# Kernel tuning notes

Measured on AMD Instinct MI355X. Metric: run time of the kernel, lower is better.

## Reference

```python
import jax, jax.numpy as jnp
import numpy as np

N = 50000
E = 800000
D_IN = 128
D_HID = 256


def setup_inputs() -> dict:
    key = jax.random.key(0)
    ks = jax.random.split(key, 9)
    x = jax.random.normal(ks[0], (N, D_IN), dtype=jnp.float32)
    edge_index = jax.random.randint(ks[1], (2, E), 0, N, dtype=jnp.int64)
    edge_weight = jax.random.uniform(ks[2], (E,), dtype=jnp.float32)
    # GCNConv params (lin: y = x @ W.T, plus bias added after aggregation)
    W1 = jax.random.normal(ks[3], (D_HID, D_IN), dtype=jnp.float32) / np.sqrt(D_IN)
    b1 = jnp.zeros((D_HID,), dtype=jnp.float32)
    W2 = jax.random.normal(ks[4], (D_IN, D_HID), dtype=jnp.float32) / np.sqrt(D_HID)
    b2 = jnp.zeros((D_IN,), dtype=jnp.float32)
    gamma = jnp.ones((D_IN,), dtype=jnp.float32)
    beta = jnp.zeros((D_IN,), dtype=jnp.float32)
    return {"x": x, "edge_index": edge_index, "edge_weight": edge_weight,
            "W1": W1, "b1": b1, "W2": W2, "b2": b2,
            "gamma": gamma, "beta": beta}


def _gcn_norm(edge_index, edge_weight, n_nodes):
    # add self loops with weight 1.0 (PyG gcn_norm default)
    loop = jnp.arange(n_nodes, dtype=edge_index.dtype)
    src = jnp.concatenate([edge_index[0], loop])
    dst = jnp.concatenate([edge_index[1], loop])
    w = jnp.concatenate([edge_weight, jnp.ones((n_nodes,), edge_weight.dtype)])
    # symmetric normalization: deg over target index
    deg = jax.ops.segment_sum(w, dst, num_segments=n_nodes)
    dinv = jnp.where(deg > 0, jax.lax.rsqrt(deg), 0.0)
    norm = dinv[src] * w * dinv[dst]
    return src, dst, norm


def _gcn_conv(x, src, dst, norm, W, b, n_nodes):
    h = x @ W.T                                    # [N, out]
    msg = h[src] * norm[:, None]                   # gather + scale [E+N, out]
    out = jax.ops.segment_sum(msg, dst, num_segments=n_nodes)
    return out + b


def reference(x, edge_index, edge_weight, W1, b1, W2, b2, gamma, beta):
    n_nodes = x.shape[0]
    src, dst, norm = _gcn_norm(edge_index, edge_weight, n_nodes)
    h = _gcn_conv(x, src, dst, norm, W1, b1, n_nodes)
    h = jax.nn.relu(h)
    h = _gcn_conv(h, src, dst, norm, W2, b2, n_nodes)
    # LayerNorm over last dim
    mu = jnp.mean(h, axis=-1, keepdims=True)
    var = jnp.mean(jnp.square(h - mu), axis=-1, keepdims=True)
    h = (h - mu) * jax.lax.rsqrt(var + 1e-5) * gamma + beta
    return h
```

## Files before the change

kernel.cpp:

```cpp
#include <hip/hip_runtime.h>

typedef unsigned short ushort_t;
typedef unsigned long long u64_t;
typedef __attribute__((ext_vector_type(8))) short short8;
typedef __attribute__((ext_vector_type(4))) float float4v;

__device__ inline float b2f(ushort_t u) {
    unsigned x = ((unsigned)u) << 16;
    return __builtin_bit_cast(float, x);
}
__device__ inline ushort_t f2b(float f) {
    unsigned x = __builtin_bit_cast(unsigned, f);
    unsigned r = (x + 0x7fffu + ((x >> 16) & 1u)) >> 16;
    return (ushort_t)r;
}

__device__ inline void load_edge(const int* __restrict__ ei, int e, int E,
                                 int& s, int& d) {
    int ec = min(e, E - 1);
    int2 c64 = ((const int2*)ei)[ec];
    unsigned long long m = __ballot(c64.y != 0);
    if (m != 0ull) {
        s = ei[ec];
        d = ei[(size_t)E + ec];
    } else {
        s = c64.x;
        d = ((const int2*)ei)[(size_t)E + ec].x;
    }
}


__global__ __launch_bounds__(256) void k_mega(const int* __restrict__ ei,
                                              const float* __restrict__ w,
                                              const float* __restrict__ x,
                                              const float* __restrict__ W1,
                                              const float* __restrict__ W2,
                                              u64_t* packed, int* __restrict__ rank,
                                              ushort_t* __restrict__ xb,
                                              ushort_t* __restrict__ W1b,
                                              ushort_t* __restrict__ W2b,
                                              int E, int Nn, int gE, int gX) {
    int b = blockIdx.x;
    if (b < gE) {
        int e = b * 256 + threadIdx.x;
        int s, d;
        load_edge(ei, e, E, s, d);
        if (e < E) {
            if ((unsigned)s < (unsigned)Nn && (unsigned)d < (unsigned)Nn) {
                unsigned fx = (unsigned)(w[e] * 16777216.0f + 0.5f);
                u64_t old = atomicAdd(packed + d, (1ull << 32) | (u64_t)fx);
                rank[e] = (int)(old >> 32);
            } else {
                rank[e] = -1;
            }
        }
    } else if (b < gE + gX) {
        int i = (b - gE) * 256 + threadIdx.x;
        if (i < Nn * 32) {
            float4v v = ((const float4v*)x)[i];
            ushort4 o;
            o.x = f2b(v[0]); o.y = f2b(v[1]); o.z = f2b(v[2]); o.w = f2b(v[3]);
            ((ushort4*)xb)[i] = o;
        }
    } else {
        int i = (b - gE - gX) * 256 + threadIdx.x;
        if (i < 32768) W1b[i] = f2b(W1[i]);
        else if (i < 65536) W2b[i - 32768] = f2b(W2[i - 32768]);
    }
}

__device__ inline int cnt_hi(const u64_t* packed, int i) {
    return ((const int*)packed)[2 * i + 1];
}


__global__ __launch_bounds__(256) void k_scan_a(const u64_t* __restrict__ packed,
                                                int* __restrict__ bsum, int Nn) {
    int b = blockIdx.x, t = threadIdx.x;
    int base = b * 2048 + t * 8;
    int s = 0;
#pragma unroll
    for (int j = 0; j < 8; ++j) { int i = base + j; if (i < Nn) s += cnt_hi(packed, i); }
#pragma unroll
    for (int off = 1; off < 64; off <<= 1) s += __shfl_xor(s, off);
    __shared__ int wsum[4];
    if ((t & 63) == 0) wsum[t >> 6] = s;
    __syncthreads();
    if (t == 0) bsum[b] = wsum[0] + wsum[1] + wsum[2] + wsum[3];
}

__global__ void k_scan_b(const int* __restrict__ bsum, int* __restrict__ bbase,
                         int nb, int* __restrict__ offs, int Nn) {
    int t = threadIdx.x;
    int own = (t < nb) ? bsum[t] : 0;
    int v = own;
#pragma unroll
    for (int off = 1; off < 64; off <<= 1) {
        int u = __shfl_up(v, off);
        if (t >= off) v += u;
    }
    if (t < nb) bbase[t] = v - own;
    if (t == 63) offs[Nn] = v;
}

__global__ __launch_bounds__(256) void k_scan_c(const u64_t* __restrict__ packed,
                                                const int* __restrict__ bbase,
                                                int* __restrict__ offs,
                                                float* __restrict__ dinv, int Nn) {
    int b = blockIdx.x, t = threadIdx.x;
    int base = b * 2048 + t * 8;
    u64_t pk[8];
    int v[8];
    int s = 0;
#pragma unroll
    for (int j = 0; j < 8; ++j) {
        int i = base + j;
        pk[j] = (i < Nn) ? packed[i] : 0ull;
        v[j] = (int)(pk[j] >> 32);
        s += v[j];
    }
    __shared__ int sd[256];
    sd[t] = s;
    __syncthreads();
    for (int off = 1; off < 256; off <<= 1) {
        int u = (t >= off) ? sd[t - off] : 0;
        __syncthreads();
        sd[t] += u;
        __syncthreads();
    }
    int pos = bbase[b] + sd[t] - s;
#pragma unroll
    for (int j = 0; j < 8; ++j) {
        int i = base + j;
        if (i < Nn) {
            offs[i] = pos; pos += v[j];
            float deg = 1.0f + (float)(unsigned)(pk[j] & 0xFFFFFFFFull) * (1.0f / 16777216.0f);
            dinv[i] = rsqrtf(deg);
        }
    }
}


__global__ void k_scatter(const int* __restrict__ ei, const float* __restrict__ w,
                          const float* __restrict__ dinv,
                          const int* __restrict__ offs,
                          const int* __restrict__ rank,
                          int2* __restrict__ edata, int E, int Nn) {
    int e = blockIdx.x * 256 + threadIdx.x;
    int s, d;
    load_edge(ei, e, E, s, d);
    if (e >= E) return;
    int r = rank[e];
    if (r < 0) return;
    int pos = offs[d] + r;
    float nw = dinv[s] * w[e] * dinv[d];
    int2 p;
    p.x = s;
    p.y = __builtin_bit_cast(int, nw);
    edata[pos] = p;
}


__device__ inline void agg_edges(const ushort_t* __restrict__ src,
                                 const int2* __restrict__ edata,
                                 int s, int e, int hl, int p, float* a) {
    int i = s;
    for (; i + 7 < e; i += 8) {
#pragma unroll
        for (int j = 0; j < 4; ++j) {
            int idx = i + p + 2 * j;
            int2 ed = edata[idx];
            float nw = __builtin_bit_cast(float, ed.y);
            ushort4 q = ((const ushort4*)(src + (size_t)ed.x * 128))[hl];
            a[0] += b2f(q.x) * nw; a[1] += b2f(q.y) * nw;
            a[2] += b2f(q.z) * nw; a[3] += b2f(q.w) * nw;
        }
    }
    for (; i < e; i += 2) {
        int idx = i + p;
        int ic = min(idx, e - 1);
        int2 ed = edata[ic];
        float nw = (idx < e) ? __builtin_bit_cast(float, ed.y) : 0.f;
        ushort4 q = ((const ushort4*)(src + (size_t)ed.x * 128))[hl];
        a[0] += b2f(q.x) * nw; a[1] += b2f(q.y) * nw;
        a[2] += b2f(q.z) * nw; a[3] += b2f(q.w) * nw;
    }
}

__global__ __launch_bounds__(256) void k_agg1(const ushort_t* __restrict__ xb,
                                              const int* __restrict__ offs,
                                              const int2* __restrict__ edata,
                                              const float* __restrict__ dinv,
                                              ushort_t* __restrict__ ax, int Nn) {
    int v = (blockIdx.x * blockDim.x + threadIdx.x) >> 6;
    int lane = threadIdx.x & 63;
    if (v >= Nn) return;
    int hl = lane & 31, p = lane >> 5;
    float a[4] = {0.f, 0.f, 0.f, 0.f};
    if (p == 0) {
        float dv = dinv[v];
        float sn = dv * dv;
        ushort4 pq = ((const ushort4*)(xb + (size_t)v * 128))[hl];
        a[0] = b2f(pq.x) * sn; a[1] = b2f(pq.y) * sn;
        a[2] = b2f(pq.z) * sn; a[3] = b2f(pq.w) * sn;
    }
    int s = offs[v], e = offs[v + 1];
    agg_edges(xb, edata, s, e, hl, p, a);
#pragma unroll
    for (int j = 0; j < 4; ++j) a[j] += __shfl_xor(a[j], 32);
    if (p == 0) {
        ushort4 o;
        o.x = f2b(a[0]); o.y = f2b(a[1]); o.z = f2b(a[2]); o.w = f2b(a[3]);
        ((ushort4*)(ax + (size_t)v * 128))[hl] = o;
    }
}


__global__ __launch_bounds__(256, 2) void k_gemm_fused(const ushort_t* __restrict__ ax,
                                                       const ushort_t* __restrict__ W1b,
                                                       const float* __restrict__ b1v,
                                                       const ushort_t* __restrict__ W2b,
                                                       ushort_t* __restrict__ h2, int Nn) {
    __shared__ ushort_t tile[64][264];
    int tid = threadIdx.x, wid = tid >> 6, lane = tid & 63;
    int m = lane & 15, q = lane >> 4;
    int blk = blockIdx.x * 64;

    short8 wf[4][4];
#pragma unroll
    for (int nt = 0; nt < 4; ++nt) {
        const ushort_t* wb = W1b + (size_t)(wid * 64 + nt * 16 + m) * 128 + q * 8;
#pragma unroll
        for (int kt = 0; kt < 4; ++kt) wf[nt][kt] = *(const short8*)(wb + kt * 32);
    }
    short8 af[4][4];
#pragma unroll
    for (int mi = 0; mi < 4; ++mi) {
        int arow = blk + mi * 16 + m;
        bool rv = arow < Nn;
        const ushort_t* ab = ax + (size_t)arow * 128 + q * 8;
#pragma unroll
        for (int kt = 0; kt < 4; ++kt)
            af[mi][kt] = rv ? *(const short8*)(ab + kt * 32) : (short8)0;
    }

    float4v acc1[4][4];
#pragma unroll
    for (int mi = 0; mi < 4; ++mi)
#pragma unroll
        for (int nt = 0; nt < 4; ++nt) acc1[mi][nt] = (float4v){0.f, 0.f, 0.f, 0.f};

#pragma unroll
    for (int kt = 0; kt < 4; ++kt)
#pragma unroll
        for (int mi = 0; mi < 4; ++mi)
#pragma unroll
            for (int nt = 0; nt < 4; ++nt)
                acc1[mi][nt] = __builtin_amdgcn_mfma_f32_16x16x32_bf16(
                    af[mi][kt], wf[nt][kt], acc1[mi][nt], 0, 0, 0);

#pragma unroll
    for (int nt = 0; nt < 4; ++nt) {
        int col = wid * 64 + nt * 16 + m;
        float bb = b1v[col];
#pragma unroll
        for (int mi = 0; mi < 4; ++mi) {
#pragma unroll
            for (int r = 0; r < 4; ++r) {
                float v = acc1[mi][nt][r] + bb;
                v = v > 0.f ? v : 0.f;
                tile[mi * 16 + q * 4 + r][col] = f2b(v);
            }
        }
    }
    __syncthreads();

    short8 w2f[2][8];
#pragma unroll
    for (int n2 = 0; n2 < 2; ++n2) {
        const ushort_t* wb = W2b + (size_t)(wid * 32 + n2 * 16 + m) * 256 + q * 8;
#pragma unroll
        for (int kt = 0; kt < 8; ++kt) w2f[n2][kt] = *(const short8*)(wb + kt * 32);
    }

    float4v acc2[4][2];
#pragma unroll
    for (int mi = 0; mi < 4; ++mi)
#pragma unroll
        for (int n2 = 0; n2 < 2; ++n2) acc2[mi][n2] = (float4v){0.f, 0.f, 0.f, 0.f};

#pragma unroll
    for (int kt = 0; kt < 8; ++kt) {
#pragma unroll
        for (int mi = 0; mi < 4; ++mi) {
            short8 a2 = *(const short8*)&tile[mi * 16 + m][kt * 32 + q * 8];
#pragma unroll
            for (int n2 = 0; n2 < 2; ++n2)
                acc2[mi][n2] = __builtin_amdgcn_mfma_f32_16x16x32_bf16(
                    a2, w2f[n2][kt], acc2[mi][n2], 0, 0, 0);
        }
    }

#pragma unroll
    for (int mi = 0; mi < 4; ++mi) {
#pragma unroll
        for (int n2 = 0; n2 < 2; ++n2) {
            int col = wid * 32 + n2 * 16 + m;
#pragma unroll
            for (int r = 0; r < 4; ++r) {
                int row = blk + mi * 16 + q * 4 + r;
                if (row < Nn) h2[(size_t)row * 128 + col] = f2b(acc2[mi][n2][r]);
            }
        }
    }
}


__global__ __launch_bounds__(256) void k_agg2_ln(const ushort_t* __restrict__ h2,
                                                 const int* __restrict__ offs,
                                                 const int2* __restrict__ edata,
                                                 const float* __restrict__ dinv,
                                                 const float* __restrict__ b2v,
                                                 const float* __restrict__ gv,
                                                 const float* __restrict__ bev,
                                                 float* __restrict__ out, int Nn) {
    int v = (blockIdx.x * blockDim.x + threadIdx.x) >> 6;
    int lane = threadIdx.x & 63;
    if (v >= Nn) return;
    int hl = lane & 31, p = lane >> 5;
    float a[4] = {0.f, 0.f, 0.f, 0.f};
    if (p == 0) {
        float dv = dinv[v];
        float sn = dv * dv;
        ushort4 pq = ((const ushort4*)(h2 + (size_t)v * 128))[hl];
        a[0] = b2f(pq.x) * sn; a[1] = b2f(pq.y) * sn;
        a[2] = b2f(pq.z) * sn; a[3] = b2f(pq.w) * sn;
    }
    int s = offs[v], e = offs[v + 1];
    agg_edges(h2, edata, s, e, hl, p, a);
#pragma unroll
    for (int j = 0; j < 4; ++j) a[j] += __shfl_xor(a[j], 32);

    int d0 = hl * 4;
#pragma unroll
    for (int j = 0; j < 4; ++j) a[j] += b2v[d0 + j];

    float ssum = a[0] + a[1] + a[2] + a[3];
    float ssq = a[0] * a[0] + a[1] * a[1] + a[2] * a[2] + a[3] * a[3];
#pragma unroll
    for (int off = 1; off < 64; off <<= 1) {
        ssum += __shfl_xor(ssum, off);
        ssq += __shfl_xor(ssq, off);
    }
    float mu = ssum * (1.0f / 256.0f);
    float var = ssq * (1.0f / 256.0f) - mu * mu;
    float r = rsqrtf(var + 1e-5f);
    if (p == 0) {
        float4v o;
#pragma unroll
        for (int j = 0; j < 4; ++j)
            o[j] = (a[j] - mu) * r * gv[d0 + j] + bev[d0 + j];
        ((float4v*)(out + (size_t)v * 128))[hl] = o;
    }
}


extern "C" void kernel_launch(void* const* d_in, const int* in_sizes, int n_in,
                              void* d_out, int out_size, void* d_ws, size_t ws_size,
                              hipStream_t stream) {
    const float* x   = (const float*)d_in[0];
    const int*   ei  = (const int*)d_in[1];
    const float* ew  = (const float*)d_in[2];
    const float* W1  = (const float*)d_in[3];
    const float* b1v = (const float*)d_in[4];
    const float* W2  = (const float*)d_in[5];
    const float* b2v = (const float*)d_in[6];
    const float* gv  = (const float*)d_in[7];
    const float* bev = (const float*)d_in[8];
    float* out = (float*)d_out;

    const int Nn = in_sizes[0] / 128;
    const int E  = in_sizes[2];

    char* base = (char*)d_ws;
    size_t off = 0;
    auto alloc = [&](size_t bytes) {
        char* p = base + off;
        off = (off + bytes + 255) & ~(size_t)255;
        return p;
    };
    u64_t*  packed = (u64_t*)alloc((size_t)Nn * 8);
    float*  dinv   = (float*)alloc((size_t)Nn * 4);
    int*    offs   = (int*)alloc((size_t)(Nn + 1) * 4);
    int*    bsum   = (int*)alloc(64 * 4);
    int*    bbase  = (int*)alloc(64 * 4);
    int*    rank   = (int*)alloc((size_t)E * 4);
    int2*   edata  = (int2*)alloc((size_t)E * 8);
    ushort_t* xb   = (ushort_t*)alloc((size_t)Nn * 128 * 2);
    ushort_t* h2   = (ushort_t*)alloc((size_t)Nn * 128 * 2);
    ushort_t* W1b  = (ushort_t*)alloc(32768 * 2);
    ushort_t* W2b  = (ushort_t*)alloc(32768 * 2);
    ushort_t* ax   = (ushort_t*)d_out;
    (void)ws_size; (void)n_in; (void)out_size;

    int gE = (E + 255) / 256;
    int gX = (Nn * 32 + 255) / 256;
    int gW = (Nn + 3) / 4;
    int gG = (Nn + 63) / 64;
    int nb = (Nn + 2047) / 2048;

    hipMemsetAsync(packed, 0, (size_t)Nn * 8, stream);
    k_mega<<<gE + gX + 256, 256, 0, stream>>>(ei, ew, x, W1, W2, packed, rank,
                                              xb, W1b, W2b, E, Nn, gE, gX);
    k_scan_a<<<nb, 256, 0, stream>>>(packed, bsum, Nn);
    k_scan_b<<<1, 64, 0, stream>>>(bsum, bbase, nb, offs, Nn);
    k_scan_c<<<nb, 256, 0, stream>>>(packed, bbase, offs, dinv, Nn);
    k_scatter<<<gE, 256, 0, stream>>>(ei, ew, dinv, offs, rank, edata, E, Nn);
    k_agg1<<<gW, 256, 0, stream>>>(xb, offs, edata, dinv, ax, Nn);
    k_gemm_fused<<<gG, 256, 0, stream>>>(ax, W1b, b1v, W2b, h2, Nn);
    k_agg2_ln<<<gW, 256, 0, stream>>>(h2, offs, edata, dinv, b2v, gv, bev, out, Nn);
}
```

Before: 262.4 us.

## Privatize degree atomics per XCD with workgroup-scope adds and per-XCD bases

Replaces the single device-wide packed degree/count array with one copy per XCD, selected by reading the hardware XCC_ID register. Each edge then does a relaxed, workgroup-scope atomic into its XCD's slice, which avoids cross-XCD coherent device-scope atomics. The edge rank now also encodes the XCD index. The scan kernels sum the eight slices and write per-XCD base offsets that the scatter kernel uses to place each edge. In exchange the memset and the scan reads grow eightfold. Correctness also depends on workgroup-scope atomics being serialized at the per-XCD L2.

Result: slower. 285.6 us (+8.8%).

```diff
diff --git a/kernel.cpp b/kernel.cpp
--- a/kernel.cpp
+++ b/kernel.cpp
@@ -4,6 +4,8 @@
 typedef unsigned long long u64_t;
 typedef __attribute__((ext_vector_type(8))) short short8;
 typedef __attribute__((ext_vector_type(4))) float float4v;
+
+#define NXCD 8
 
 __device__ inline float b2f(ushort_t u) {
     unsigned x = ((unsigned)u) << 16;
@@ -45,11 +47,16 @@
         int e = b * 256 + threadIdx.x;
         int s, d;
         load_edge(ei, e, E, s, d);
+        int xcc;
+        asm("s_getreg_b32 %0, hwreg(HW_REG_XCC_ID)" : "=s"(xcc));
+        xcc &= (NXCD - 1);
         if (e < E) {
             if ((unsigned)s < (unsigned)Nn && (unsigned)d < (unsigned)Nn) {
                 unsigned fx = (unsigned)(w[e] * 16777216.0f + 0.5f);
-                u64_t old = atomicAdd(packed + d, (1ull << 32) | (u64_t)fx);
-                rank[e] = (int)(old >> 32);
+                u64_t old = __hip_atomic_fetch_add(
+                    packed + (size_t)xcc * Nn + d, (1ull << 32) | (u64_t)fx,
+                    __ATOMIC_RELAXED, __HIP_MEMORY_SCOPE_WORKGROUP);
+                rank[e] = (int)(((unsigned)(old >> 32)) << 3) | xcc;
             } else {
                 rank[e] = -1;
             }
@@ -69,7 +76,7 @@
     }
 }
 
-__device__ inline int cnt_hi(const u64_t* packed, int i) {
+__device__ inline int cnt_hi(const u64_t* packed, size_t i) {
     return ((const int*)packed)[2 * i + 1];
 }
 
@@ -80,7 +87,13 @@
     int base = b * 2048 + t * 8;
     int s = 0;
 #pragma unroll
-    for (int j = 0; j < 8; ++j) { int i = base + j; if (i < Nn) s += cnt_hi(packed, i); }
+    for (int j = 0; j < 8; ++j) {
+        int i = base + j;
+        if (i < Nn) {
+#pragma unroll
+            for (int c = 0; c < NXCD; ++c) s += cnt_hi(packed, (size_t)c * Nn + i);
+        }
+    }
 #pragma unroll
     for (int off = 1; off < 64; off <<= 1) s += __shfl_xor(s, off);
     __shared__ int wsum[4];
@@ -106,18 +119,18 @@
 __global__ __launch_bounds__(256) void k_scan_c(const u64_t* __restrict__ packed,
                                                 const int* __restrict__ bbase,
                                                 int* __restrict__ offs,
-                                                float* __restrict__ dinv, int Nn) {
+                                                float* __restrict__ dinv,
+                                                int* __restrict__ cbase, int Nn) {
     int b = blockIdx.x, t = threadIdx.x;
     int base = b * 2048 + t * 8;
-    u64_t pk[8];
-    int v[8];
     int s = 0;
 #pragma unroll
     for (int j = 0; j < 8; ++j) {
         int i = base + j;
-        pk[j] = (i < Nn) ? packed[i] : 0ull;
-        v[j] = (int)(pk[j] >> 32);
-        s += v[j];
+        if (i < Nn) {
+#pragma unroll
+            for (int c = 0; c < NXCD; ++c) s += cnt_hi(packed, (size_t)c * Nn + i);
+        }
     }
     __shared__ int sd[256];
     sd[t] = s;
@@ -133,8 +146,18 @@
     for (int j = 0; j < 8; ++j) {
         int i = base + j;
         if (i < Nn) {
-            offs[i] = pos; pos += v[j];
-            float deg = 1.0f + (float)(unsigned)(pk[j] & 0xFFFFFFFFull) * (1.0f / 16777216.0f);
+            offs[i] = pos;
+            u64_t wsum = 0;
+            int run = pos;
+#pragma unroll
+            for (int c = 0; c < NXCD; ++c) {
+                u64_t pk = packed[(size_t)c * Nn + i];
+                cbase[(size_t)c * Nn + i] = run;
+                run += (int)(pk >> 32);
+                wsum += (pk & 0xFFFFFFFFull);
+            }
+            pos = run;
+            float deg = 1.0f + (float)wsum * (1.0f / 16777216.0f);
             dinv[i] = rsqrtf(deg);
         }
     }
@@ -143,16 +166,18 @@
 
 __global__ void k_scatter(const int* __restrict__ ei, const float* __restrict__ w,
                           const float* __restrict__ dinv,
-                          const int* __restrict__ offs,
+                          const int* __restrict__ cbase,
                           const int* __restrict__ rank,
                           int2* __restrict__ edata, int E, int Nn) {
     int e = blockIdx.x * 256 + threadIdx.x;
     int s, d;
     load_edge(ei, e, E, s, d);
     if (e >= E) return;
-    int r = rank[e];
-    if (r < 0) return;
-    int pos = offs[d] + r;
+    int r3 = rank[e];
+    if (r3 < 0) return;
+    int c = r3 & (NXCD - 1);
+    int r = r3 >> 3;
+    int pos = cbase[(size_t)c * Nn + d] + r;
     float nw = dinv[s] * w[e] * dinv[d];
     int2 p;
     p.x = s;
@@ -389,7 +414,8 @@
         off = (off + bytes + 255) & ~(size_t)255;
         return p;
     };
-    u64_t*  packed = (u64_t*)alloc((size_t)Nn * 8);
+    u64_t*  packed = (u64_t*)alloc((size_t)NXCD * Nn * 8);
+    int*    cbase  = (int*)alloc((size_t)NXCD * Nn * 4);
     float*  dinv   = (float*)alloc((size_t)Nn * 4);
     int*    offs   = (int*)alloc((size_t)(Nn + 1) * 4);
     int*    bsum   = (int*)alloc(64 * 4);
@@ -409,13 +435,13 @@
     int gG = (Nn + 63) / 64;
     int nb = (Nn + 2047) / 2048;
 
-    hipMemsetAsync(packed, 0, (size_t)Nn * 8, stream);
+    hipMemsetAsync(packed, 0, (size_t)NXCD * Nn * 8, stream);
     k_mega<<<gE + gX + 256, 256, 0, stream>>>(ei, ew, x, W1, W2, packed, rank,
                                               xb, W1b, W2b, E, Nn, gE, gX);
     k_scan_a<<<nb, 256, 0, stream>>>(packed, bsum, Nn);
     k_scan_b<<<1, 64, 0, stream>>>(bsum, bbase, nb, offs, Nn);
-    k_scan_c<<<nb, 256, 0, stream>>>(packed, bbase, offs, dinv, Nn);
-    k_scatter<<<gE, 256, 0, stream>>>(ei, ew, dinv, offs, rank, edata, E, Nn);
+    k_scan_c<<<nb, 256, 0, stream>>>(packed, bbase, offs, dinv, cbase, Nn);
+    k_scatter<<<gE, 256, 0, stream>>>(ei, ew, dinv, cbase, rank, edata, E, Nn);
     k_agg1<<<gW, 256, 0, stream>>>(xb, offs, edata, dinv, ax, Nn);
     k_gemm_fused<<<gG, 256, 0, stream>>>(ax, W1b, b1v, W2b, h2, Nn);
     k_agg2_ln<<<gW, 256, 0, stream>>>(h2, offs, edata, dinv, b2v, gv, bev, out, Nn);
```
